# Kernel tuning notes

Measured on AMD Instinct MI355X. Metric: run time of the kernel, lower is better.

Reference implementation:

```python
import jax, jax.numpy as jnp
import numpy as np

N = 50000
E = 800000
IN_DIM, HID_DIM, EMB_DIM = 128, 256, 128


def _sage_conv(x, src, dst, Wp, bp, Wl, bl, Wr):
    # PyG SAGEConv(project=True, aggr='max'):
    #   x_proj = relu(x @ Wp + bp)            # projection before message passing
    #   aggr   = scatter_max(x_proj[src] -> dst)  (empty segments -> 0)
    #   out    = aggr @ Wl + bl + x @ Wr      # lin_l(aggr) + lin_r(root)
    x_proj = jax.nn.relu(x @ Wp + bp)                      # [N, in]
    msg = x_proj[src]                                      # [E, in] gather
    aggr = jax.ops.segment_max(msg, dst, num_segments=N)   # [N, in] scatter-max
    aggr = jnp.where(jnp.isneginf(aggr), 0.0, aggr)        # empty neighborhoods -> 0
    return aggr @ Wl + bl + x @ Wr


def setup_inputs() -> dict:
    key = jax.random.key(0)
    ks = jax.random.split(key, 12)
    s = 0.05
    return {
        "x": jax.random.normal(ks[0], (N, IN_DIM), dtype=jnp.float32),
        "edge_index": jax.random.randint(ks[1], (2, E), 0, N, dtype=jnp.int64),
        # layer 1 params
        "Wp1": jax.random.normal(ks[2], (IN_DIM, IN_DIM), dtype=jnp.float32) * s,
        "bp1": jnp.zeros((IN_DIM,), dtype=jnp.float32),
        "Wl1": jax.random.normal(ks[3], (IN_DIM, HID_DIM), dtype=jnp.float32) * s,
        "bl1": jnp.zeros((HID_DIM,), dtype=jnp.float32),
        "Wr1": jax.random.normal(ks[4], (IN_DIM, HID_DIM), dtype=jnp.float32) * s,
        # layer 2 params
        "Wp2": jax.random.normal(ks[5], (HID_DIM, HID_DIM), dtype=jnp.float32) * s,
        "bp2": jnp.zeros((HID_DIM,), dtype=jnp.float32),
        "Wl2": jax.random.normal(ks[6], (HID_DIM, EMB_DIM), dtype=jnp.float32) * s,
        "bl2": jnp.zeros((EMB_DIM,), dtype=jnp.float32),
        "Wr2": jax.random.normal(ks[7], (HID_DIM, EMB_DIM), dtype=jnp.float32) * s,
    }


def reference(x, edge_index, Wp1, bp1, Wl1, bl1, Wr1, Wp2, bp2, Wl2, bl2, Wr2):
    src, dst = edge_index[0], edge_index[1]
    h = jax.nn.relu(_sage_conv(x, src, dst, Wp1, bp1, Wl1, bl1, Wr1))
    h = jax.nn.relu(_sage_conv(h, src, dst, Wp2, bp2, Wl2, bl2, Wr2))
    return h
```

## Files before the change

### kernel.cpp

```cpp
#include <hip/hip_runtime.h>


typedef __attribute__((ext_vector_type(8))) short short8;
typedef __attribute__((ext_vector_type(4))) float f32x4;

#define ADJ_CAP 64
#define EPB 2048

__device__ __forceinline__ unsigned short f2bf(float f) {
    unsigned int u = __float_as_uint(f);
    u += 0x7fffu + ((u >> 16) & 1u);
    return (unsigned short)(u >> 16);
}

__device__ __forceinline__ unsigned int pkmax(unsigned int a, unsigned int b) {
    unsigned int r;
    asm("v_pk_max_u16 %0, %1, %2" : "=v"(r) : "v"(a), "v"(b));
    return r;
}

__device__ __forceinline__ short8 pack8(const float4 f0, const float4 f1) {
    union { unsigned short u[8]; short8 v; } r;
    r.u[0] = f2bf(f0.x); r.u[1] = f2bf(f0.y); r.u[2] = f2bf(f0.z); r.u[3] = f2bf(f0.w);
    r.u[4] = f2bf(f1.x); r.u[5] = f2bf(f1.y); r.u[6] = f2bf(f1.z); r.u[7] = f2bf(f1.w);
    return r.v;
}

__global__ __launch_bounds__(256) void pack_all_kernel(
    const float* __restrict__ Wp1, const float* __restrict__ Wl1,
    const float* __restrict__ Wr1, const float* __restrict__ Wp2,
    const float* __restrict__ Wl2, const float* __restrict__ Wr2,
    unsigned short* __restrict__ P0, unsigned short* __restrict__ P1,
    unsigned short* __restrict__ P2, unsigned short* __restrict__ P3,
    unsigned short* __restrict__ P4, unsigned short* __restrict__ P5)
{
    const int idx = blockIdx.x * 256 + threadIdx.x;
    const float* W; unsigned short* P; int Nc, local;
    if      (idx <  16384) { W = Wp1; P = P0; Nc = 128; local = idx; }
    else if (idx <  49152) { W = Wl1; P = P1; Nc = 256; local = idx - 16384; }
    else if (idx <  81920) { W = Wr1; P = P2; Nc = 256; local = idx - 49152; }
    else if (idx < 147456) { W = Wp2; P = P3; Nc = 256; local = idx - 81920; }
    else if (idx < 180224) { W = Wl2; P = P4; Nc = 128; local = idx - 147456; }
    else if (idx < 212992) { W = Wr2; P = P5; Nc = 128; local = idx - 180224; }
    else return;
    const int k = local / Nc, c = local % Nc;
    P[((size_t)(k >> 3) * Nc + c) * 8 + (k & 7)] = f2bf(W[local]);
}

__global__ __launch_bounds__(256) void build_adj_sliced(
    const int* __restrict__ src, const int* __restrict__ dst,
    int* __restrict__ deg, unsigned short* __restrict__ padj,
    int E, int M)
{
    const int slice = blockIdx.x & 7;
    const int chunk = blockIdx.x >> 3;
    const int sliceSz = (M + 7) >> 3;
    const int lo = slice * sliceSz;
    const int hi = min(M, lo + sliceSz);
    const int base = chunk * EPB;
#pragma unroll
    for (int k = 0; k < EPB; k += 256) {
        const int e = base + k + (int)threadIdx.x;
        if (e < E) {
            const int d = dst[e];
            const int s = src[e];
            if (d >= lo && d < hi) {
                const int pos = atomicAdd(&deg[d], 1);
                if (pos < ADJ_CAP)
                    padj[(size_t)d * ADJ_CAP + pos] = (unsigned short)s;
            }
        }
    }
}

__global__ __launch_bounds__(256) void gemm_proj_f32(
    const float* __restrict__ A,
    const unsigned short* __restrict__ W,
    const float* __restrict__ bias,
    unsigned short* __restrict__ outp,
    int M)
{
    constexpr int K = 128, N = 128, BK = 32, LDK = BK + 8;
    __shared__ unsigned short As[64 * LDK];

    const int tid  = threadIdx.x;
    const int lane = tid & 63;
    const int wave = tid >> 6;
    const int fr   = lane & 15;
    const int g    = lane >> 4;
    const int bm   = blockIdx.x * 64;
    const int wr   = (wave >> 1) * 32;
    const int wc   = (wave & 1) * 64;

    const f32x4 zero = {0.f, 0.f, 0.f, 0.f};
    f32x4 acc[2][4];
#pragma unroll
    for (int m = 0; m < 2; ++m)
#pragma unroll
        for (int n = 0; n < 4; ++n) acc[m][n] = zero;

    for (int kt = 0; kt < K / BK; ++kt) {
        if (kt) __syncthreads();
        {
            const int r = tid >> 2, q = tid & 3;
            const int gm = min(bm + r, M - 1);
            const float4 f0 = *reinterpret_cast<const float4*>(A + (size_t)gm * K + kt * BK + q * 8);
            const float4 f1 = *reinterpret_cast<const float4*>(A + (size_t)gm * K + kt * BK + q * 8 + 4);
            *reinterpret_cast<short8*>(&As[r * LDK + q * 8]) = pack8(f0, f1);
        }
        __syncthreads();
        short8 af[2];
#pragma unroll
        for (int m = 0; m < 2; ++m)
            af[m] = *reinterpret_cast<const short8*>(&As[(wr + m * 16 + fr) * LDK + g * 8]);
#pragma unroll
        for (int n = 0; n < 4; ++n) {
            const short8 bf = *reinterpret_cast<const short8*>(
                W + ((size_t)(kt * 4 + g) * N + wc + n * 16 + fr) * 8);
#pragma unroll
            for (int m = 0; m < 2; ++m)
                acc[m][n] = __builtin_amdgcn_mfma_f32_16x16x32_bf16(af[m], bf, acc[m][n], 0, 0, 0);
        }
    }

    float bv[4];
#pragma unroll
    for (int n = 0; n < 4; ++n) bv[n] = bias[wc + n * 16 + fr];
#pragma unroll
    for (int m = 0; m < 2; ++m)
#pragma unroll
        for (int j = 0; j < 4; ++j) {
            const int row = bm + wr + m * 16 + g * 4 + j;
            if (row < M)
#pragma unroll
                for (int n = 0; n < 4; ++n)
                    outp[(size_t)row * N + wc + n * 16 + fr] =
                        f2bf(fmaxf(acc[m][n][j] + bv[n], 0.f));
        }
}

template<int D>
__global__ __launch_bounds__(256) void gather_max_bf16(
    const unsigned short* __restrict__ p, const unsigned short* __restrict__ padj,
    const int* __restrict__ deg, unsigned short* __restrict__ aggr, int n)
{
    const int node = (blockIdx.x * 256 + threadIdx.x) >> 6;
    const int lane = threadIdx.x & 63;
    if (node >= n) return;
    int d = deg[node];
    if (d > ADJ_CAP) d = ADJ_CAP;
    const unsigned short* __restrict__ a = padj + (size_t)node * ADJ_CAP;

    if (D == 128) {
        const int q  = lane >> 4;
        const int ll = lane & 15;
        uint4 acc = make_uint4(0u, 0u, 0u, 0u);
        for (int e = 0; e < d; e += 16) {
            const int i0 = min(e + q,      d - 1);
            const int i1 = min(e + 4 + q,  d - 1);
            const int i2 = min(e + 8 + q,  d - 1);
            const int i3 = min(e + 12 + q, d - 1);
            const int r0 = a[i0], r1 = a[i1], r2 = a[i2], r3 = a[i3];
            const uint4 v0 = *reinterpret_cast<const uint4*>(p + (size_t)r0 * 128 + ll * 8);
            const uint4 v1 = *reinterpret_cast<const uint4*>(p + (size_t)r1 * 128 + ll * 8);
            const uint4 v2 = *reinterpret_cast<const uint4*>(p + (size_t)r2 * 128 + ll * 8);
            const uint4 v3 = *reinterpret_cast<const uint4*>(p + (size_t)r3 * 128 + ll * 8);
            acc.x = pkmax(acc.x, pkmax(pkmax(v0.x, v1.x), pkmax(v2.x, v3.x)));
            acc.y = pkmax(acc.y, pkmax(pkmax(v0.y, v1.y), pkmax(v2.y, v3.y)));
            acc.z = pkmax(acc.z, pkmax(pkmax(v0.z, v1.z), pkmax(v2.z, v3.z)));
            acc.w = pkmax(acc.w, pkmax(pkmax(v0.w, v1.w), pkmax(v2.w, v3.w)));
        }
        acc.x = pkmax(acc.x, (unsigned int)__shfl_xor((int)acc.x, 16, 64));
        acc.y = pkmax(acc.y, (unsigned int)__shfl_xor((int)acc.y, 16, 64));
        acc.z = pkmax(acc.z, (unsigned int)__shfl_xor((int)acc.z, 16, 64));
        acc.w = pkmax(acc.w, (unsigned int)__shfl_xor((int)acc.w, 16, 64));
        acc.x = pkmax(acc.x, (unsigned int)__shfl_xor((int)acc.x, 32, 64));
        acc.y = pkmax(acc.y, (unsigned int)__shfl_xor((int)acc.y, 32, 64));
        acc.z = pkmax(acc.z, (unsigned int)__shfl_xor((int)acc.z, 32, 64));
        acc.w = pkmax(acc.w, (unsigned int)__shfl_xor((int)acc.w, 32, 64));
        if (lane < 16)
            *reinterpret_cast<uint4*>(aggr + (size_t)node * 128 + ll * 8) = acc;
    } else {
        const int h  = lane >> 5;
        const int ll = lane & 31;
        uint4 acc = make_uint4(0u, 0u, 0u, 0u);
        for (int e = 0; e < d; e += 16) {
            const int i0 = min(e + h,      d - 1);
            const int i1 = min(e + 2 + h,  d - 1);
            const int i2 = min(e + 4 + h,  d - 1);
            const int i3 = min(e + 6 + h,  d - 1);
            const int i4 = min(e + 8 + h,  d - 1);
            const int i5 = min(e + 10 + h, d - 1);
            const int i6 = min(e + 12 + h, d - 1);
            const int i7 = min(e + 14 + h, d - 1);
            const int r0 = a[i0], r1 = a[i1], r2 = a[i2], r3 = a[i3];
            const int r4 = a[i4], r5 = a[i5], r6 = a[i6], r7 = a[i7];
            const uint4 v0 = *reinterpret_cast<const uint4*>(p + (size_t)r0 * 256 + ll * 8);
            const uint4 v1 = *reinterpret_cast<const uint4*>(p + (size_t)r1 * 256 + ll * 8);
            const uint4 v2 = *reinterpret_cast<const uint4*>(p + (size_t)r2 * 256 + ll * 8);
            const uint4 v3 = *reinterpret_cast<const uint4*>(p + (size_t)r3 * 256 + ll * 8);
            const uint4 v4 = *reinterpret_cast<const uint4*>(p + (size_t)r4 * 256 + ll * 8);
            const uint4 v5 = *reinterpret_cast<const uint4*>(p + (size_t)r5 * 256 + ll * 8);
            const uint4 v6 = *reinterpret_cast<const uint4*>(p + (size_t)r6 * 256 + ll * 8);
            const uint4 v7 = *reinterpret_cast<const uint4*>(p + (size_t)r7 * 256 + ll * 8);
            acc.x = pkmax(acc.x, pkmax(pkmax(pkmax(v0.x, v1.x), pkmax(v2.x, v3.x)),
                                        pkmax(pkmax(v4.x, v5.x), pkmax(v6.x, v7.x))));
            acc.y = pkmax(acc.y, pkmax(pkmax(pkmax(v0.y, v1.y), pkmax(v2.y, v3.y)),
                                        pkmax(pkmax(v4.y, v5.y), pkmax(v6.y, v7.y))));
            acc.z = pkmax(acc.z, pkmax(pkmax(pkmax(v0.z, v1.z), pkmax(v2.z, v3.z)),
                                        pkmax(pkmax(v4.z, v5.z), pkmax(v6.z, v7.z))));
            acc.w = pkmax(acc.w, pkmax(pkmax(pkmax(v0.w, v1.w), pkmax(v2.w, v3.w)),
                                        pkmax(pkmax(v4.w, v5.w), pkmax(v6.w, v7.w))));
        }
        acc.x = pkmax(acc.x, (unsigned int)__shfl_xor((int)acc.x, 32, 64));
        acc.y = pkmax(acc.y, (unsigned int)__shfl_xor((int)acc.y, 32, 64));
        acc.z = pkmax(acc.z, (unsigned int)__shfl_xor((int)acc.z, 32, 64));
        acc.w = pkmax(acc.w, (unsigned int)__shfl_xor((int)acc.w, 32, 64));
        if (lane < 32)
            *reinterpret_cast<uint4*>(aggr + (size_t)node * 256 + ll * 8) = acc;
    }
}

__global__ __launch_bounds__(256) void tail1_kernel(
    const unsigned short* __restrict__ a1,
    const float* __restrict__ x,
    const unsigned short* __restrict__ Wl,
    const unsigned short* __restrict__ Wr,
    const float* __restrict__ bl,
    const unsigned short* __restrict__ Wp2,
    const float* __restrict__ bp2,
    unsigned short* __restrict__ h1,
    unsigned short* __restrict__ p2,
    int M)
{
    constexpr int LDK = 136;
    constexpr int LDH = 264;
    __shared__ unsigned short As[32 * LDK];
    __shared__ unsigned short Hs[32 * LDH];

    const int tid  = threadIdx.x;
    const int lane = tid & 63;
    const int wave = tid >> 6;
    const int fr   = lane & 15;
    const int g    = lane >> 4;
    const int bm   = blockIdx.x * 32;
    const int wc   = wave * 64;

    const f32x4 zero = {0.f, 0.f, 0.f, 0.f};
    f32x4 acc[2][4];
#pragma unroll
    for (int m = 0; m < 2; ++m)
#pragma unroll
        for (int n = 0; n < 4; ++n) acc[m][n] = zero;

#pragma unroll
    for (int c = 0; c < 2; ++c) {
        const int t = tid + c * 256;
        const int r = t >> 4, q = t & 15;
        const int gm = min(bm + r, M - 1);
        *reinterpret_cast<short8*>(&As[r * LDK + q * 8]) =
            *reinterpret_cast<const short8*>(a1 + (size_t)gm * 128 + q * 8);
    }
    __syncthreads();
#pragma unroll
    for (int kt = 0; kt < 4; ++kt) {
        short8 af[2];
#pragma unroll
        for (int m = 0; m < 2; ++m)
            af[m] = *reinterpret_cast<const short8*>(&As[(m * 16 + fr) * LDK + kt * 32 + g * 8]);
#pragma unroll
        for (int n = 0; n < 4; ++n) {
            const short8 bf = *reinterpret_cast<const short8*>(
                Wl + ((size_t)(kt * 4 + g) * 256 + wc + n * 16 + fr) * 8);
#pragma unroll
            for (int m = 0; m < 2; ++m)
                acc[m][n] = __builtin_amdgcn_mfma_f32_16x16x32_bf16(af[m], bf, acc[m][n], 0, 0, 0);
        }
    }
    __syncthreads();
#pragma unroll
    for (int c = 0; c < 2; ++c) {
        const int t = tid + c * 256;
        const int r = t >> 4, q = t & 15;
        const int gm = min(bm + r, M - 1);
        const float4 f0 = *reinterpret_cast<const float4*>(x + (size_t)gm * 128 + q * 8);
        const float4 f1 = *reinterpret_cast<const float4*>(x + (size_t)gm * 128 + q * 8 + 4);
        *reinterpret_cast<short8*>(&As[r * LDK + q * 8]) = pack8(f0, f1);
    }
    __syncthreads();
#pragma unroll
    for (int kt = 0; kt < 4; ++kt) {
        short8 af[2];
#pragma unroll
        for (int m = 0; m < 2; ++m)
            af[m] = *reinterpret_cast<const short8*>(&As[(m * 16 + fr) * LDK + kt * 32 + g * 8]);
#pragma unroll
        for (int n = 0; n < 4; ++n) {
            const short8 bf = *reinterpret_cast<const short8*>(
                Wr + ((size_t)(kt * 4 + g) * 256 + wc + n * 16 + fr) * 8);
#pragma unroll
            for (int m = 0; m < 2; ++m)
                acc[m][n] = __builtin_amdgcn_mfma_f32_16x16x32_bf16(af[m], bf, acc[m][n], 0, 0, 0);
        }
    }

    {
        float bv[4];
#pragma unroll
        for (int n = 0; n < 4; ++n) bv[n] = bl[wc + n * 16 + fr];
#pragma unroll
        for (int m = 0; m < 2; ++m)
#pragma unroll
            for (int j = 0; j < 4; ++j) {
                const int rl = m * 16 + g * 4 + j;
#pragma unroll
                for (int n = 0; n < 4; ++n) {
                    const unsigned short hb = f2bf(fmaxf(acc[m][n][j] + bv[n], 0.f));
                    Hs[rl * LDH + wc + n * 16 + fr] = hb;
                    if (bm + rl < M)
                        h1[(size_t)(bm + rl) * 256 + wc + n * 16 + fr] = hb;
                }
            }
    }
    __syncthreads();

#pragma unroll
    for (int m = 0; m < 2; ++m)
#pragma unroll
        for (int n = 0; n < 4; ++n) acc[m][n] = zero;
#pragma unroll
    for (int kt = 0; kt < 8; ++kt) {
        short8 af[2];
#pragma unroll
        for (int m = 0; m < 2; ++m)
            af[m] = *reinterpret_cast<const short8*>(&Hs[(m * 16 + fr) * LDH + kt * 32 + g * 8]);
#pragma unroll
        for (int n = 0; n < 4; ++n) {
            const short8 bf = *reinterpret_cast<const short8*>(
                Wp2 + ((size_t)(kt * 4 + g) * 256 + wc + n * 16 + fr) * 8);
#pragma unroll
            for (int m = 0; m < 2; ++m)
                acc[m][n] = __builtin_amdgcn_mfma_f32_16x16x32_bf16(af[m], bf, acc[m][n], 0, 0, 0);
        }
    }
    {
        float bv[4];
#pragma unroll
        for (int n = 0; n < 4; ++n) bv[n] = bp2[wc + n * 16 + fr];
#pragma unroll
        for (int m = 0; m < 2; ++m)
#pragma unroll
            for (int j = 0; j < 4; ++j) {
                const int row = bm + m * 16 + g * 4 + j;
                if (row < M)
#pragma unroll
                    for (int n = 0; n < 4; ++n)
                        p2[(size_t)row * 256 + wc + n * 16 + fr] =
                            f2bf(fmaxf(acc[m][n][j] + bv[n], 0.f));
            }
    }
}

__global__ __launch_bounds__(256) void tail2_kernel(
    const unsigned short* __restrict__ a2,
    const unsigned short* __restrict__ h1,
    const unsigned short* __restrict__ Wl,
    const unsigned short* __restrict__ Wr,
    const float* __restrict__ bl,
    float* __restrict__ out, int M)
{
    constexpr int LDK = 264;
    __shared__ unsigned short As[32 * LDK];

    const int tid  = threadIdx.x;
    const int lane = tid & 63;
    const int wave = tid >> 6;
    const int fr   = lane & 15;
    const int g    = lane >> 4;
    const int bm   = blockIdx.x * 32;
    const int wc   = wave * 32;

    const f32x4 zero = {0.f, 0.f, 0.f, 0.f};
    f32x4 acc[2][2];
#pragma unroll
    for (int m = 0; m < 2; ++m)
#pragma unroll
        for (int n = 0; n < 2; ++n) acc[m][n] = zero;

#pragma unroll
    for (int ph = 0; ph < 2; ++ph) {
        const unsigned short* __restrict__ P = ph ? h1 : a2;
        const unsigned short* __restrict__ W = ph ? Wr : Wl;
        if (ph) __syncthreads();
#pragma unroll
        for (int c = 0; c < 4; ++c) {
            const int t = tid + c * 256;
            const int r = t >> 5, q = t & 31;
            const int gm = min(bm + r, M - 1);
            *reinterpret_cast<short8*>(&As[r * LDK + q * 8]) =
                *reinterpret_cast<const short8*>(P + (size_t)gm * 256 + q * 8);
        }
        __syncthreads();
#pragma unroll
        for (int kt = 0; kt < 8; ++kt) {
            short8 af[2];
#pragma unroll
            for (int m = 0; m < 2; ++m)
                af[m] = *reinterpret_cast<const short8*>(&As[(m * 16 + fr) * LDK + kt * 32 + g * 8]);
#pragma unroll
            for (int n = 0; n < 2; ++n) {
                const short8 bf = *reinterpret_cast<const short8*>(
                    W + ((size_t)(kt * 4 + g) * 128 + wc + n * 16 + fr) * 8);
#pragma unroll
                for (int m = 0; m < 2; ++m)
                    acc[m][n] = __builtin_amdgcn_mfma_f32_16x16x32_bf16(af[m], bf, acc[m][n], 0, 0, 0);
            }
        }
    }

    float bv[2];
#pragma unroll
    for (int n = 0; n < 2; ++n) bv[n] = bl[wc + n * 16 + fr];
#pragma unroll
    for (int m = 0; m < 2; ++m)
#pragma unroll
        for (int j = 0; j < 4; ++j) {
            const int row = bm + m * 16 + g * 4 + j;
            if (row < M)
#pragma unroll
                for (int n = 0; n < 2; ++n)
                    out[(size_t)row * 128 + wc + n * 16 + fr] =
                        fmaxf(acc[m][n][j] + bv[n], 0.f);
        }
}

extern "C" void kernel_launch(void* const* d_in, const int* in_sizes, int n_in,
                              void* d_out, int out_size, void* d_ws, size_t ws_size,
                              hipStream_t stream)
{
    const float* x   = (const float*)d_in[0];
    const int*   ei  = (const int*)d_in[1];
    const float* Wp1 = (const float*)d_in[2];
    const float* bp1 = (const float*)d_in[3];
    const float* Wl1 = (const float*)d_in[4];
    const float* bl1 = (const float*)d_in[5];
    const float* Wr1 = (const float*)d_in[6];
    const float* Wp2 = (const float*)d_in[7];
    const float* bp2 = (const float*)d_in[8];
    const float* Wl2 = (const float*)d_in[9];
    const float* bl2 = (const float*)d_in[10];
    const float* Wr2 = (const float*)d_in[11];
    float* out = (float*)d_out;

    const int M = in_sizes[0] / 128;
    const int E = in_sizes[1] / 2;
    const int* src = ei;
    const int* dst = ei + E;

    unsigned short* ws  = (unsigned short*)d_ws;
    unsigned short* p1b = ws;
    unsigned short* a1b = p1b + (size_t)M * 128;
    unsigned short* h1b = a1b + (size_t)M * 128;
    unsigned short* p2b = h1b + (size_t)M * 256;
    unsigned short* a2b = p2b + (size_t)M * 256;
    unsigned short* wpk = a2b + (size_t)M * 256;
    unsigned short* Wp1p = wpk;
    unsigned short* Wl1p = Wp1p + 128 * 128;
    unsigned short* Wr1p = Wl1p + 128 * 256;
    unsigned short* Wp2p = Wr1p + 128 * 256;
    unsigned short* Wl2p = Wp2p + 256 * 256;
    unsigned short* Wr2p = Wl2p + 256 * 128;
    unsigned short* endu = Wr2p + 256 * 128;
    size_t off = ((size_t)(endu - ws) * 2 + 127) & ~(size_t)127;
    unsigned short* padj = (unsigned short*)((char*)d_ws + off);
    size_t off2 = (off + (size_t)M * ADJ_CAP * 2 + 127) & ~(size_t)127;
    int* deg = (int*)((char*)d_ws + off2);

    const dim3 blk(256);
    const int gb = (M + 3) / 4;
    const int mb64 = (M + 63) / 64;
    const int mb32 = (M + 31) / 32;
    const int nChunks = (E + EPB - 1) / EPB;

    pack_all_kernel<<<(212992 + 255) / 256, blk, 0, stream>>>(
        Wp1, Wl1, Wr1, Wp2, Wl2, Wr2, Wp1p, Wl1p, Wr1p, Wp2p, Wl2p, Wr2p);
    hipMemsetAsync(deg, 0, (size_t)M * sizeof(int), stream);
    build_adj_sliced<<<8 * nChunks, blk, 0, stream>>>(src, dst, deg, padj, E, M);
    gemm_proj_f32<<<mb64, blk, 0, stream>>>(x, Wp1p, bp1, p1b, M);

    gather_max_bf16<128><<<gb, blk, 0, stream>>>(p1b, padj, deg, a1b, M);
    tail1_kernel<<<mb32, blk, 0, stream>>>(
        a1b, x, Wl1p, Wr1p, bl1, Wp2p, bp2, h1b, p2b, M);

    gather_max_bf16<256><<<gb, blk, 0, stream>>>(p2b, padj, deg, a2b, M);
    tail2_kernel<<<mb32, blk, 0, stream>>>(
        a2b, h1b, Wl2p, Wr2p, bl2, out, M);
}
```

Measured before the change: 198.5 us.

## Store degree in adjacency slot 0, load row once, concatenate layer-1 weights

The adjacency row now keeps its neighbour count in slot 0. A fused finalize pass inside the projection kernel writes that count, so the gather kernels load the whole 64-entry row in one coalesced read and hand out neighbour indices with shuffles instead of separate deg and per-edge index loads. Layer 1's Wl and Wr are packed into one 256-row matrix so tail1 runs a single K=256 MFMA loop over [aggr|x] staged in shared memory, dropping the second staging pass and barriers. Neighbour capacity drops from 64 to 63 per node, which only matters if some node has a degree that high.

```diff
diff --git a/kernel.cpp b/kernel.cpp
--- a/kernel.cpp
+++ b/kernel.cpp
@@ -31,19 +31,19 @@
     const float* __restrict__ Wr1, const float* __restrict__ Wp2,
     const float* __restrict__ Wl2, const float* __restrict__ Wr2,
     unsigned short* __restrict__ P0, unsigned short* __restrict__ P1,
-    unsigned short* __restrict__ P2, unsigned short* __restrict__ P3,
+    unsigned short* __restrict__ P3,
     unsigned short* __restrict__ P4, unsigned short* __restrict__ P5)
 {
     const int idx = blockIdx.x * 256 + threadIdx.x;
-    const float* W; unsigned short* P; int Nc, local;
+    const float* W; unsigned short* P; int Nc, local, kofs = 0;
     if      (idx <  16384) { W = Wp1; P = P0; Nc = 128; local = idx; }
     else if (idx <  49152) { W = Wl1; P = P1; Nc = 256; local = idx - 16384; }
-    else if (idx <  81920) { W = Wr1; P = P2; Nc = 256; local = idx - 49152; }
+    else if (idx <  81920) { W = Wr1; P = P1; Nc = 256; local = idx - 49152; kofs = 128; }
     else if (idx < 147456) { W = Wp2; P = P3; Nc = 256; local = idx - 81920; }
     else if (idx < 180224) { W = Wl2; P = P4; Nc = 128; local = idx - 147456; }
     else if (idx < 212992) { W = Wr2; P = P5; Nc = 128; local = idx - 180224; }
     else return;
-    const int k = local / Nc, c = local % Nc;
+    const int k = local / Nc + kofs, c = local % Nc;
     P[((size_t)(k >> 3) * Nc + c) * 8 + (k & 7)] = f2bf(W[local]);
 }
 
@@ -66,20 +66,28 @@
             const int s = src[e];
             if (d >= lo && d < hi) {
                 const int pos = atomicAdd(&deg[d], 1);
-                if (pos < ADJ_CAP)
-                    padj[(size_t)d * ADJ_CAP + pos] = (unsigned short)s;
+                if (pos < ADJ_CAP - 1)
+                    padj[(size_t)d * ADJ_CAP + 1 + pos] = (unsigned short)s;
             }
         }
     }
 }
 
-__global__ __launch_bounds__(256) void gemm_proj_f32(
+__global__ __launch_bounds__(256) void projfin_kernel(
     const float* __restrict__ A,
     const unsigned short* __restrict__ W,
     const float* __restrict__ bias,
     unsigned short* __restrict__ outp,
-    int M)
-{
+    int M, int mbProj,
+    const int* __restrict__ deg, unsigned short* __restrict__ padj)
+{
+    if ((int)blockIdx.x >= mbProj) {
+        const int i = (blockIdx.x - mbProj) * 256 + threadIdx.x;
+        if (i < M)
+            padj[(size_t)i * ADJ_CAP] = (unsigned short)min(deg[i], ADJ_CAP - 1);
+        return;
+    }
+
     constexpr int K = 128, N = 128, BK = 32, LDK = BK + 8;
     __shared__ unsigned short As[64 * LDK];
 
@@ -142,25 +150,23 @@
 template<int D>
 __global__ __launch_bounds__(256) void gather_max_bf16(
     const unsigned short* __restrict__ p, const unsigned short* __restrict__ padj,
-    const int* __restrict__ deg, unsigned short* __restrict__ aggr, int n)
+    unsigned short* __restrict__ aggr, int n)
 {
     const int node = (blockIdx.x * 256 + threadIdx.x) >> 6;
     const int lane = threadIdx.x & 63;
     if (node >= n) return;
-    int d = deg[node];
-    if (d > ADJ_CAP) d = ADJ_CAP;
-    const unsigned short* __restrict__ a = padj + (size_t)node * ADJ_CAP;
+    const int av  = (int)padj[(size_t)node * ADJ_CAP + lane];
+    const int cnt = __shfl(av, 0, 64);
 
     if (D == 128) {
         const int q  = lane >> 4;
         const int ll = lane & 15;
         uint4 acc = make_uint4(0u, 0u, 0u, 0u);
-        for (int e = 0; e < d; e += 16) {
-            const int i0 = min(e + q,      d - 1);
-            const int i1 = min(e + 4 + q,  d - 1);
-            const int i2 = min(e + 8 + q,  d - 1);
-            const int i3 = min(e + 12 + q, d - 1);
-            const int r0 = a[i0], r1 = a[i1], r2 = a[i2], r3 = a[i3];
+        for (int e = 1; e <= cnt; e += 16) {
+            const int r0 = __shfl(av, min(e + q,      cnt), 64);
+            const int r1 = __shfl(av, min(e + 4 + q,  cnt), 64);
+            const int r2 = __shfl(av, min(e + 8 + q,  cnt), 64);
+            const int r3 = __shfl(av, min(e + 12 + q, cnt), 64);
             const uint4 v0 = *reinterpret_cast<const uint4*>(p + (size_t)r0 * 128 + ll * 8);
             const uint4 v1 = *reinterpret_cast<const uint4*>(p + (size_t)r1 * 128 + ll * 8);
             const uint4 v2 = *reinterpret_cast<const uint4*>(p + (size_t)r2 * 128 + ll * 8);
@@ -184,17 +190,15 @@
         const int h  = lane >> 5;
         const int ll = lane & 31;
         uint4 acc = make_uint4(0u, 0u, 0u, 0u);
-        for (int e = 0; e < d; e += 16) {
-            const int i0 = min(e + h,      d - 1);
-            const int i1 = min(e + 2 + h,  d - 1);
-            const int i2 = min(e + 4 + h,  d - 1);
-            const int i3 = min(e + 6 + h,  d - 1);
-            const int i4 = min(e + 8 + h,  d - 1);
-            const int i5 = min(e + 10 + h, d - 1);
-            const int i6 = min(e + 12 + h, d - 1);
-            const int i7 = min(e + 14 + h, d - 1);
-            const int r0 = a[i0], r1 = a[i1], r2 = a[i2], r3 = a[i3];
-            const int r4 = a[i4], r5 = a[i5], r6 = a[i6], r7 = a[i7];
+        for (int e = 1; e <= cnt; e += 16) {
+            const int r0 = __shfl(av, min(e + h,      cnt), 64);
+            const int r1 = __shfl(av, min(e + 2 + h,  cnt), 64);
+            const int r2 = __shfl(av, min(e + 4 + h,  cnt), 64);
+            const int r3 = __shfl(av, min(e + 6 + h,  cnt), 64);
+            const int r4 = __shfl(av, min(e + 8 + h,  cnt), 64);
+            const int r5 = __shfl(av, min(e + 10 + h, cnt), 64);
+            const int r6 = __shfl(av, min(e + 12 + h, cnt), 64);
+            const int r7 = __shfl(av, min(e + 14 + h, cnt), 64);
             const uint4 v0 = *reinterpret_cast<const uint4*>(p + (size_t)r0 * 256 + ll * 8);
             const uint4 v1 = *reinterpret_cast<const uint4*>(p + (size_t)r1 * 256 + ll * 8);
             const uint4 v2 = *reinterpret_cast<const uint4*>(p + (size_t)r2 * 256 + ll * 8);
@@ -224,8 +228,7 @@
 __global__ __launch_bounds__(256) void tail1_kernel(
     const unsigned short* __restrict__ a1,
     const float* __restrict__ x,
-    const unsigned short* __restrict__ Wl,
-    const unsigned short* __restrict__ Wr,
+    const unsigned short* __restrict__ Wcat,
     const float* __restrict__ bl,
     const unsigned short* __restrict__ Wp2,
     const float* __restrict__ bp2,
@@ -233,9 +236,7 @@
     unsigned short* __restrict__ p2,
     int M)
 {
-    constexpr int LDK = 136;
     constexpr int LDH = 264;
-    __shared__ unsigned short As[32 * LDK];
     __shared__ unsigned short Hs[32 * LDH];
 
     const int tid  = threadIdx.x;
@@ -254,55 +255,37 @@
         for (int n = 0; n < 4; ++n) acc[m][n] = zero;
 
 #pragma unroll
-    for (int c = 0; c < 2; ++c) {
+    for (int c = 0; c < 4; ++c) {
         const int t = tid + c * 256;
-        const int r = t >> 4, q = t & 15;
+        const int r = t >> 5, q = t & 31;
         const int gm = min(bm + r, M - 1);
-        *reinterpret_cast<short8*>(&As[r * LDK + q * 8]) =
-            *reinterpret_cast<const short8*>(a1 + (size_t)gm * 128 + q * 8);
+        short8 v;
+        if (q < 16) {
+            v = *reinterpret_cast<const short8*>(a1 + (size_t)gm * 128 + q * 8);
+        } else {
+            const float4 f0 = *reinterpret_cast<const float4*>(x + (size_t)gm * 128 + (q - 16) * 8);
+            const float4 f1 = *reinterpret_cast<const float4*>(x + (size_t)gm * 128 + (q - 16) * 8 + 4);
+            v = pack8(f0, f1);
+        }
+        *reinterpret_cast<short8*>(&Hs[r * LDH + q * 8]) = v;
     }
     __syncthreads();
 #pragma unroll
-    for (int kt = 0; kt < 4; ++kt) {
+    for (int kt = 0; kt < 8; ++kt) {
         short8 af[2];
 #pragma unroll
         for (int m = 0; m < 2; ++m)
-            af[m] = *reinterpret_cast<const short8*>(&As[(m * 16 + fr) * LDK + kt * 32 + g * 8]);
+            af[m] = *reinterpret_cast<const short8*>(&Hs[(m * 16 + fr) * LDH + kt * 32 + g * 8]);
 #pragma unroll
         for (int n = 0; n < 4; ++n) {
             const short8 bf = *reinterpret_cast<const short8*>(
-                Wl + ((size_t)(kt * 4 + g) * 256 + wc + n * 16 + fr) * 8);
+                Wcat + ((size_t)(kt * 4 + g) * 256 + wc + n * 16 + fr) * 8);
 #pragma unroll
             for (int m = 0; m < 2; ++m)
                 acc[m][n] = __builtin_amdgcn_mfma_f32_16x16x32_bf16(af[m], bf, acc[m][n], 0, 0, 0);
         }
     }
     __syncthreads();
-#pragma unroll
-    for (int c = 0; c < 2; ++c) {
-        const int t = tid + c * 256;
-        const int r = t >> 4, q = t & 15;
-        const int gm = min(bm + r, M - 1);
-        const float4 f0 = *reinterpret_cast<const float4*>(x + (size_t)gm * 128 + q * 8);
-        const float4 f1 = *reinterpret_cast<const float4*>(x + (size_t)gm * 128 + q * 8 + 4);
-        *reinterpret_cast<short8*>(&As[r * LDK + q * 8]) = pack8(f0, f1);
-    }
-    __syncthreads();
-#pragma unroll
-    for (int kt = 0; kt < 4; ++kt) {
-        short8 af[2];
-#pragma unroll
-        for (int m = 0; m < 2; ++m)
-            af[m] = *reinterpret_cast<const short8*>(&As[(m * 16 + fr) * LDK + kt * 32 + g * 8]);
-#pragma unroll
-        for (int n = 0; n < 4; ++n) {
-            const short8 bf = *reinterpret_cast<const short8*>(
-                Wr + ((size_t)(kt * 4 + g) * 256 + wc + n * 16 + fr) * 8);
-#pragma unroll
-            for (int m = 0; m < 2; ++m)
-                acc[m][n] = __builtin_amdgcn_mfma_f32_16x16x32_bf16(af[m], bf, acc[m][n], 0, 0, 0);
-        }
-    }
 
     {
         float bv[4];
@@ -464,13 +447,12 @@
     unsigned short* p2b = h1b + (size_t)M * 256;
     unsigned short* a2b = p2b + (size_t)M * 256;
     unsigned short* wpk = a2b + (size_t)M * 256;
-    unsigned short* Wp1p = wpk;
-    unsigned short* Wl1p = Wp1p + 128 * 128;
-    unsigned short* Wr1p = Wl1p + 128 * 256;
-    unsigned short* Wp2p = Wr1p + 128 * 256;
-    unsigned short* Wl2p = Wp2p + 256 * 256;
-    unsigned short* Wr2p = Wl2p + 256 * 128;
-    unsigned short* endu = Wr2p + 256 * 128;
+    unsigned short* Wp1p  = wpk;
+    unsigned short* Wcat1 = Wp1p + 128 * 128;
+    unsigned short* Wp2p  = Wcat1 + 256 * 256;
+    unsigned short* Wl2p  = Wp2p + 256 * 256;
+    unsigned short* Wr2p  = Wl2p + 256 * 128;
+    unsigned short* endu  = Wr2p + 256 * 128;
     size_t off = ((size_t)(endu - ws) * 2 + 127) & ~(size_t)127;
     unsigned short* padj = (unsigned short*)((char*)d_ws + off);
     size_t off2 = (off + (size_t)M * ADJ_CAP * 2 + 127) & ~(size_t)127;
@@ -480,19 +462,21 @@
     const int gb = (M + 3) / 4;
     const int mb64 = (M + 63) / 64;
     const int mb32 = (M + 31) / 32;
+    const int fb = (M + 255) / 256;
     const int nChunks = (E + EPB - 1) / EPB;
 
     pack_all_kernel<<<(212992 + 255) / 256, blk, 0, stream>>>(
-        Wp1, Wl1, Wr1, Wp2, Wl2, Wr2, Wp1p, Wl1p, Wr1p, Wp2p, Wl2p, Wr2p);
+        Wp1, Wl1, Wr1, Wp2, Wl2, Wr2, Wp1p, Wcat1, Wp2p, Wl2p, Wr2p);
     hipMemsetAsync(deg, 0, (size_t)M * sizeof(int), stream);
     build_adj_sliced<<<8 * nChunks, blk, 0, stream>>>(src, dst, deg, padj, E, M);
-    gemm_proj_f32<<<mb64, blk, 0, stream>>>(x, Wp1p, bp1, p1b, M);
-
-    gather_max_bf16<128><<<gb, blk, 0, stream>>>(p1b, padj, deg, a1b, M);
+    projfin_kernel<<<mb64 + fb, blk, 0, stream>>>(
+        x, Wp1p, bp1, p1b, M, mb64, deg, padj);
+
+    gather_max_bf16<128><<<gb, blk, 0, stream>>>(p1b, padj, a1b, M);
     tail1_kernel<<<mb32, blk, 0, stream>>>(
-        a1b, x, Wl1p, Wr1p, bl1, Wp2p, bp2, h1b, p2b, M);
-
-    gather_max_bf16<256><<<gb, blk, 0, stream>>>(p2b, padj, deg, a2b, M);
+        a1b, x, Wcat1, bl1, Wp2p, bp2, h1b, p2b, M);
+
+    gather_max_bf16<256><<<gb, blk, 0, stream>>>(p2b, padj, a2b, M);
     tail2_kernel<<<mb32, blk, 0, stream>>>(
         a2b, h1b, Wl2p, Wr2p, bl2, out, M);
 }
```

Result: faster. 194.0 us, median of 2 (-2.2%).
